# Kernel tuning notes

Hardware: AMD Instinct MI355X
Metric: run time of the kernel (lower is better)

Reference implementation:

```python
import jax, jax.numpy as jnp
import numpy as np

EPS_LN = 1e-5
EPS_BN = 1e-5

B, S, N, F, H, E, L = 8, 16, 1024, 16, 128, 32768, 4


def _layernorm(h, g, b):
    mu = h.mean(-1, keepdims=True)
    var = ((h - mu) ** 2).mean(-1, keepdims=True)
    return (h - mu) / jnp.sqrt(var + EPS_LN) * g + b


def setup_inputs() -> dict:
    key = jax.random.key(0)
    ks = iter(jax.random.split(key, 40))
    nrm = lambda shape, s=0.05: jax.random.normal(next(ks), shape, dtype=jnp.float32) * s
    inp = {
        'x': jax.random.normal(next(ks), (B, S, N, F), dtype=jnp.float32),
        'edge_index': jax.random.randint(next(ks), (2, E), 0, N, dtype=jnp.int32),
        'edge_weights': jax.random.uniform(next(ks), (E,), dtype=jnp.float32),
        'edge_features': jax.random.normal(next(ks), (E, 1), dtype=jnp.float32),
        # input projection: Linear(F,H) + LayerNorm(H)
        'w_in': nrm((F, H), 1.0 / np.sqrt(F)), 'b_in': nrm((H,)),
        'ln_in_g': jnp.ones((H,), jnp.float32), 'ln_in_b': jnp.zeros((H,), jnp.float32),
        # edge feature proj: Linear(1,H) -> ReLU -> Linear(H,1) -> Sigmoid
        'w_e1': nrm((1, H), 1.0), 'b_e1': nrm((H,)),
        'w_e2': nrm((H, 1), 1.0 / np.sqrt(H)), 'b_e2': nrm((1,)),
        # L GCN layers (weight [H,H], bias [H]) + BatchNorm1d affine params
        'gcn_w': nrm((L, H, H), 1.0 / np.sqrt(H)), 'gcn_b': nrm((L, H)),
        'bn_g': jnp.ones((L, H), jnp.float32), 'bn_b': jnp.zeros((L, H), jnp.float32),
        # 2-layer LSTM (PyTorch gate order i,f,g,o)
        'lstm_wih': nrm((2, 4 * H, H), 1.0 / np.sqrt(H)), 'lstm_whh': nrm((2, 4 * H, H), 1.0 / np.sqrt(H)),
        'lstm_bih': nrm((2, 4 * H)), 'lstm_bhh': nrm((2, 4 * H)),
        # output projection: Linear(H,H//2) + LayerNorm + Linear(H//2,1)
        'w_o1': nrm((H, H // 2), 1.0 / np.sqrt(H)), 'b_o1': nrm((H // 2,)),
        'ln_o_g': jnp.ones((H // 2,), jnp.float32), 'ln_o_b': jnp.zeros((H // 2,), jnp.float32),
        'w_o2': nrm((H // 2, 1), 1.0 / np.sqrt(H // 2)), 'b_o2': nrm((1,)),
    }
    return inp


def _forward(x, edge_index, edge_weights, edge_features,
             w_in, b_in, ln_in_g, ln_in_b, w_e1, b_e1, w_e2, b_e2,
             gcn_w, gcn_b, bn_g, bn_b,
             lstm_wih, lstm_whh, lstm_bih, lstm_bhh,
             w_o1, b_o1, ln_o_g, ln_o_b, w_o2, b_o2):
    Bs, Ss, Ns, Fs = x.shape
    BN = Bs * Ns
    # edge attention gating of edge weights
    e = jax.nn.relu(edge_features @ w_e1 + b_e1)
    att = jax.nn.sigmoid(e @ w_e2 + b_e2)[:, 0]            # [E]
    ew = edge_weights * att
    # input projection (dropout = identity in eval)
    h0 = jax.nn.relu(_layernorm(x @ w_in + b_in, ln_in_g, ln_in_b))   # [B,S,N,H]
    xf = h0.reshape(Bs * Ss, Ns, H)
    # replicate original slicing x[t:t+B] on the flattened (B*S) axis
    idx = jnp.arange(Ss)[:, None] + jnp.arange(Bs)[None, :]           # [S,B]
    hs = xf[idx].reshape(Ss, BN, H)                                   # [S,B*N,H]
    # GCN normalization (shared across timesteps): self-loops over all B*N nodes
    src = jnp.concatenate([edge_index[0], jnp.arange(BN, dtype=edge_index.dtype)])
    dst = jnp.concatenate([edge_index[1], jnp.arange(BN, dtype=edge_index.dtype)])
    w_sl = jnp.concatenate([ew, jnp.ones((BN,), ew.dtype)])
    deg = jax.ops.segment_sum(w_sl, dst, num_segments=BN)
    dis = jnp.where(deg > 0, jax.lax.rsqrt(jnp.where(deg > 0, deg, 1.0)), 0.0)
    norm = dis[src] * w_sl * dis[dst]                                  # [E+BN]
    # eval-mode BatchNorm (running mean 0, var 1)
    bn_scale = bn_g / np.sqrt(1.0 + EPS_BN)

    def gcn_block(h):                                                  # [BN,H]
        for l in range(L):
            identity = h
            hw = h @ gcn_w[l]
            m = jax.ops.segment_sum(hw[src] * norm[:, None], dst, num_segments=BN) + gcn_b[l]
            h = jax.nn.relu(m * bn_scale[l] + bn_b[l]) + identity
        return h

    hs = jax.vmap(gcn_block)(hs)                                       # [S,B*N,H]
    xt = jnp.transpose(hs.reshape(Ss, Bs, Ns, H), (1, 0, 2, 3))        # [B,S,N,H]
    # LSTM over the time axis for each (b,n) node sequence
    seq = jnp.transpose(xt, (0, 2, 1, 3)).reshape(BN, Ss, H)           # [B*N,S,H]

    def lstm_layer(seq, wih, whh, bih, bhh):
        def step(carry, xt):
            hprev, cprev = carry
            gates = xt @ wih.T + hprev @ whh.T + bih + bhh
            i, f, g, o = jnp.split(gates, 4, axis=-1)
            c = jax.nn.sigmoid(f) * cprev + jax.nn.sigmoid(i) * jnp.tanh(g)
            hn = jax.nn.sigmoid(o) * jnp.tanh(c)
            return (hn, c), hn
        z = jnp.zeros((seq.shape[0], H), seq.dtype)
        _, ys = jax.lax.scan(step, (z, z), jnp.swapaxes(seq, 0, 1))
        return jnp.swapaxes(ys, 0, 1)                                  # [B*N,S,H]

    y = lstm_layer(seq, lstm_wih[0], lstm_whh[0], lstm_bih[0], lstm_bhh[0])
    y = lstm_layer(y, lstm_wih[1], lstm_whh[1], lstm_bih[1], lstm_bhh[1])
    y = y[:, -1].reshape(Bs, Ns, H)
    z = jax.nn.relu(_layernorm(y @ w_o1 + b_o1, ln_o_g, ln_o_b))
    out = z @ w_o2 + b_o2                                              # [B,N,1]
    return out[..., None]                                              # [B,N,1,1]


def reference(x, edge_index, edge_weights, edge_features,
              w_in, b_in, ln_in_g, ln_in_b, w_e1, b_e1, w_e2, b_e2,
              gcn_w, gcn_b, bn_g, bn_b,
              lstm_wih, lstm_whh, lstm_bih, lstm_bhh,
              w_o1, b_o1, ln_o_g, ln_o_b, w_o2, b_o2):
    return _forward(x, edge_index, edge_weights, edge_features,
                    w_in, b_in, ln_in_g, ln_in_b, w_e1, b_e1, w_e2, b_e2,
                    gcn_w, gcn_b, bn_g, bn_b,
                    lstm_wih, lstm_whh, lstm_bih, lstm_bhh,
                    w_o1, b_o1, ln_o_g, ln_o_b, w_o2, b_o2)
```

## Files before the change

kernel.cpp:

```cpp
#include <hip/hip_runtime.h>
#include <cstdint>

#define EPS 1e-5f

typedef unsigned short ushort_t;
typedef __bf16 bf16x8 __attribute__((ext_vector_type(8)));
typedef float f32x4 __attribute__((ext_vector_type(4)));

#define GLD16(gp, lp) __builtin_amdgcn_global_load_lds( \
    (const __attribute__((address_space(1))) void*)(gp), \
    (__attribute__((address_space(3))) void*)(lp), 16, 0, 0)

__device__ __forceinline__ float sigm(float x) { return 1.f / (1.f + expf(-x)); }
__device__ __forceinline__ unsigned short f2bf(float f) {
    unsigned int u = __builtin_bit_cast(unsigned int, f);
    return (unsigned short)((u + 0x7fffu + ((u >> 16) & 1u)) >> 16);
}
__device__ __forceinline__ float bf2f(unsigned short s) {
    unsigned int u = ((unsigned int)s) << 16;
    return __builtin_bit_cast(float, u);
}
__device__ __forceinline__ float sigm_fast(float x) {
    float t = __builtin_amdgcn_exp2f(-1.44269504f * x);
    return __builtin_amdgcn_rcpf(1.f + t);
}
__device__ __forceinline__ float tanh_fast(float x) {
    float xc = fminf(fmaxf(x, -15.f), 15.f);
    float t = __builtin_amdgcn_exp2f(-2.88539008f * xc);
    return (1.f - t) * __builtin_amdgcn_rcpf(1.f + t);
}

__global__ __launch_bounds__(256) void edge_att_deg(const float* __restrict__ ef,
                                                    const float* __restrict__ we1,
                                                    const float* __restrict__ be1,
                                                    const float* __restrict__ we2,
                                                    const float* __restrict__ be2,
                                                    const float* __restrict__ ewin,
                                                    const int* __restrict__ dst,
                                                    float* __restrict__ ew,
                                                    float* __restrict__ deg) {
    int e = blockIdx.x * blockDim.x + threadIdx.x;
    if (e >= 32768) return;
    float x = ef[e];
    float acc = 0.f;
    for (int h = 0; h < 128; ++h) {
        float v = fmaxf(x * we1[h] + be1[h], 0.f);
        acc += v * we2[h];
    }
    float wv = ewin[e] * sigm(acc + be2[0]);
    ew[e] = wv;
    atomicAdd(&deg[dst[e]], wv);
}
__global__ __launch_bounds__(256) void make_dis(float* __restrict__ deg) {
    int i = blockIdx.x * blockDim.x + threadIdx.x;
    if (i < 1024) { float d = deg[i] + 1.0f; deg[i] = (d > 0.f) ? rsqrtf(d) : 0.f; }
}
__global__ __launch_bounds__(256) void scatterA(const int* __restrict__ src,
                                                const int* __restrict__ dst,
                                                const float* __restrict__ ew,
                                                const float* __restrict__ dis,
                                                float* __restrict__ A) {
    int e = blockIdx.x * blockDim.x + threadIdx.x;
    if (e >= 32768) return;
    int s = src[e], d = dst[e];
    atomicAdd(&A[d * 1024 + s], dis[s] * ew[e] * dis[d]);
}

__global__ __launch_bounds__(256) void convF2B(const float* __restrict__ s,
                                               ushort_t* __restrict__ d, int n) {
    int i = blockIdx.x * blockDim.x + threadIdx.x;
    if (i < n) d[i] = f2bf(s[i]);
}
__global__ __launch_bounds__(256) void conv_all(const float* __restrict__ gcnw,
                                                const float* __restrict__ wih,
                                                const float* __restrict__ whh,
                                                const float* __restrict__ bih,
                                                const float* __restrict__ bhh,
                                                ushort_t* __restrict__ gcnwT,
                                                ushort_t* __restrict__ wgi,
                                                ushort_t* __restrict__ wgh,
                                                float* __restrict__ bsg) {
    int i = blockIdx.x * 256 + threadIdx.x;
    if (i < 65536) {
        int l = i >> 14, rem = i & 16383, in = rem >> 7, outc = rem & 127;
        gcnwT[l * 16384 + outc * 128 + in] = f2bf(gcnw[i]);
        return;
    }
    int j = i - 65536;
    if (j < 131072) {
        int l = j >> 16, rem = j & 65535, c = rem >> 7, kx = rem & 127;
        int g = (c >> 4) & 3, h = (c >> 6) * 16 + (c & 15);
        int src = (l * 512 + g * 128 + h) * 128 + kx;
        wgi[j] = f2bf(wih[src]);
        wgh[j] = f2bf(whh[src]);
        return;
    }
    int b = j - 131072;
    if (b < 1024) {
        int l = b >> 9, c = b & 511;
        int g = (c >> 4) & 3, h = (c >> 6) * 16 + (c & 15);
        int src = l * 512 + g * 128 + h;
        bsg[b] = bih[src] + bhh[src];
    }
}

__global__ __launch_bounds__(256) void in_proj_ln(const float* __restrict__ x,
                                                  const float* __restrict__ w,
                                                  const float* __restrict__ bias,
                                                  const float* __restrict__ g,
                                                  const float* __restrict__ be,
                                                  ushort_t* __restrict__ hA,
                                                  ushort_t* __restrict__ hB) {
    int row = blockIdx.x * 4 + (threadIdx.x >> 6);
    int lane = threadIdx.x & 63;
    int k = row >> 10, n = row & 1023;
    float xv = x[(int64_t)row * 16 + (lane & 15)];
    float a0 = bias[lane], a1 = bias[lane + 64];
#pragma unroll
    for (int f = 0; f < 16; ++f) {
        float xf = __shfl(xv, f, 16);
        a0 += xf * w[f * 128 + lane];
        a1 += xf * w[f * 128 + lane + 64];
    }
    float s = a0 + a1;
#pragma unroll
    for (int off = 1; off < 64; off <<= 1) s += __shfl_xor(s, off, 64);
    float mu = s * (1.f / 128.f);
    float d0 = a0 - mu, d1 = a1 - mu;
    float vs = d0 * d0 + d1 * d1;
#pragma unroll
    for (int off = 1; off < 64; off <<= 1) vs += __shfl_xor(vs, off, 64);
    float rstd = rsqrtf(vs * (1.f / 128.f) + EPS);
    float v0 = fmaxf(d0 * rstd * g[lane] + be[lane], 0.f);
    float v1 = fmaxf(d1 * rstd * g[lane + 64] + be[lane + 64], 0.f);
    int64_t idx = ((int64_t)k * 1024 + n) * 128 + lane;
    ushort_t b0 = f2bf(v0), b1v = f2bf(v1);
    if (k < 16) { hA[idx] = b0; hA[idx + 64] = b1v; }
    hB[idx] = b0; hB[idx + 64] = b1v;
}

__global__ __launch_bounds__(256) void gemm_feat_t(const ushort_t* __restrict__ hA,
                                                   const ushort_t* __restrict__ Wt,
                                                   ushort_t* __restrict__ hwT) {
    __shared__ __align__(16) char AsB[32768];
    __shared__ __align__(16) char BsB[32768];
    const int tid = threadIdx.x, lane = tid & 63, wid = tid >> 6;
    const int wr = wid >> 1, wc = wid & 1, q = lane >> 4, l15 = lane & 15;
    const int t = blockIdx.y;
    const int row0 = blockIdx.x * 128;
    const ushort_t* Ap = hA + ((int64_t)t * 1024 + row0) * 128;
    f32x4 acc[4][4];
#pragma unroll
    for (int m = 0; m < 4; ++m)
#pragma unroll
        for (int n = 0; n < 4; ++n) acc[m][n] = f32x4{0.f, 0.f, 0.f, 0.f};
#pragma unroll
    for (int i = 0; i < 8; ++i) {
        int id = i * 256 + tid; int r = id >> 4, sg = id & 15;
        uint4 va = *(const uint4*)(Ap + r * 128 + sg * 8);
        *(uint4*)(AsB + r * 256 + ((sg * 16) ^ ((r & 7) << 4))) = va;
        uint4 vb = *(const uint4*)(Wt + r * 128 + sg * 8);
        *(uint4*)(BsB + r * 256 + ((sg * 16) ^ ((r & 7) << 4))) = vb;
    }
    __syncthreads();
#pragma unroll
    for (int kk = 0; kk < 4; ++kk) {
        bf16x8 af[4], bfr[4];
#pragma unroll
        for (int m = 0; m < 4; ++m) {
            int row = wr * 64 + m * 16 + l15;
            af[m] = __builtin_bit_cast(bf16x8,
                *(const uint4*)(AsB + row * 256 + ((kk * 64 + q * 16) ^ ((row & 7) << 4))));
        }
#pragma unroll
        for (int n = 0; n < 4; ++n) {
            int col = wc * 64 + n * 16 + l15;
            bfr[n] = __builtin_bit_cast(bf16x8,
                *(const uint4*)(BsB + col * 256 + ((kk * 64 + q * 16) ^ ((col & 7) << 4))));
        }
#pragma unroll
        for (int m = 0; m < 4; ++m)
#pragma unroll
            for (int n = 0; n < 4; ++n)
                acc[m][n] = __builtin_amdgcn_mfma_f32_16x16x32_bf16(af[m], bfr[n], acc[m][n], 0, 0, 0);
    }
#pragma unroll
    for (int m = 0; m < 4; ++m) {
        int bn = row0 + wr * 64 + m * 16 + q * 4;
#pragma unroll
        for (int n = 0; n < 4; ++n) {
            int col = wc * 64 + n * 16 + l15;
            ushort4 u;
            u.x = f2bf(acc[m][n][0]); u.y = f2bf(acc[m][n][1]);
            u.z = f2bf(acc[m][n][2]); u.w = f2bf(acc[m][n][3]);
            *(ushort4*)(hwT + ((int64_t)t * 128 + col) * 1024 + bn) = u;
        }
    }
}

__global__ __launch_bounds__(256) void gcn_layer(ushort_t* __restrict__ hA,
                                                 ushort_t* __restrict__ hB,
                                                 const ushort_t* __restrict__ Wt,
                                                 const ushort_t* __restrict__ Abf,
                                                 const ushort_t* __restrict__ hwT,
                                                 const float* __restrict__ dis,
                                                 const float* __restrict__ gcnb,
                                                 const float* __restrict__ bng,
                                                 const float* __restrict__ bnb) {
    __shared__ __align__(16) char AsB[16384];
    __shared__ __align__(16) char BsB[32768];
    const int tid = threadIdx.x, lane = tid & 63, wid = tid >> 6;
    const int wr = wid >> 1, wc = wid & 1, q = lane >> 4, l15 = lane & 15;
    const int bx = blockIdx.x;
    const bool adj = bx < 256;
    const int lb = adj ? bx : bx - 256;
    const int tt = lb >> 4;
    const int n0 = (lb & 15) * 64;
    ushort_t* Ap = (adj ? hA : hB) + ((int64_t)tt * 1024 + n0) * 128;

#pragma unroll
    for (int i = 0; i < 4; ++i) {
        int id = i * 256 + tid; int r = id >> 4, sg = id & 15;
        uint4 va = *(const uint4*)(Ap + r * 128 + sg * 8);
        *(uint4*)(AsB + r * 256 + ((sg * 16) ^ ((r & 7) << 4))) = va;
    }
#pragma unroll
    for (int i = 0; i < 8; ++i) {
        int id = i * 256 + tid; int r = id >> 4, sg = id & 15;
        uint4 vb = *(const uint4*)(Wt + r * 128 + sg * 8);
        *(uint4*)(BsB + r * 256 + ((sg * 16) ^ ((r & 7) << 4))) = vb;
    }
    __syncthreads();

    f32x4 accF[2][4];
#pragma unroll
    for (int m = 0; m < 2; ++m)
#pragma unroll
        for (int n = 0; n < 4; ++n) accF[m][n] = f32x4{0.f, 0.f, 0.f, 0.f};
#pragma unroll
    for (int kk = 0; kk < 4; ++kk) {
        bf16x8 af[2], bfr[4];
#pragma unroll
        for (int m = 0; m < 2; ++m) {
            int row = wr * 32 + m * 16 + l15;
            af[m] = __builtin_bit_cast(bf16x8,
                *(const uint4*)(AsB + row * 256 + ((kk * 64 + q * 16) ^ ((row & 7) << 4))));
        }
#pragma unroll
        for (int n = 0; n < 4; ++n) {
            int col = wc * 64 + n * 16 + l15;
            bfr[n] = __builtin_bit_cast(bf16x8,
                *(const uint4*)(BsB + col * 256 + ((kk * 64 + q * 16) ^ ((col & 7) << 4))));
        }
#pragma unroll
        for (int m = 0; m < 2; ++m)
#pragma unroll
            for (int n = 0; n < 4; ++n)
                accF[m][n] = __builtin_amdgcn_mfma_f32_16x16x32_bf16(af[m], bfr[n], accF[m][n], 0, 0, 0);
    }

    f32x4 accA[2][4];
#pragma unroll
    for (int m = 0; m < 2; ++m)
#pragma unroll
        for (int n = 0; n < 4; ++n) accA[m][n] = f32x4{0.f, 0.f, 0.f, 0.f};
    if (adj) {
        const int rl8 = lane >> 3;
        const int sgg = (lane & 7) ^ rl8;
        for (int k0 = 0; k0 < 1024; k0 += 64) {
            __syncthreads();
#pragma unroll
            for (int i = 0; i < 2; ++i) {
                int r = i * 32 + wid * 8 + rl8;
                GLD16(Abf + (int64_t)(n0 + r) * 1024 + k0 + sgg * 8,
                      BsB + (i * 32 + wid * 8) * 128);
            }
#pragma unroll
            for (int i = 0; i < 4; ++i) {
                int r = i * 32 + wid * 8 + rl8;
                GLD16(hwT + (int64_t)tt * 131072 + (int64_t)r * 1024 + k0 + sgg * 8,
                      BsB + 8192 + (i * 32 + wid * 8) * 128);
            }
            __syncthreads();
#pragma unroll
            for (int kk = 0; kk < 2; ++kk) {
                bf16x8 af2[2], bf2[4];
#pragma unroll
                for (int m = 0; m < 2; ++m) {
                    int row = wr * 32 + m * 16 + l15;
                    af2[m] = __builtin_bit_cast(bf16x8,
                        *(const uint4*)(BsB + row * 128 + ((kk * 64 + q * 16) ^ ((row & 7) << 4))));
                }
#pragma unroll
                for (int n = 0; n < 4; ++n) {
                    int col = wc * 64 + n * 16 + l15;
                    bf2[n] = __builtin_bit_cast(bf16x8,
                        *(const uint4*)(BsB + 8192 + col * 128 + ((kk * 64 + q * 16) ^ ((col & 7) << 4))));
                }
#pragma unroll
                for (int m = 0; m < 2; ++m)
#pragma unroll
                    for (int n = 0; n < 4; ++n)
                        accA[m][n] = __builtin_amdgcn_mfma_f32_16x16x32_bf16(af2[m], bf2[n], accA[m][n], 0, 0, 0);
            }
        }
    }
    __syncthreads();

    const float rs = rsqrtf(1.f + EPS);
#pragma unroll
    for (int n = 0; n < 4; ++n) {
        int col = wc * 64 + n * 16 + l15;
        float gb = gcnb[col], sc = bng[col] * rs, bb = bnb[col];
        int seg16 = (col >> 3) * 16, wb = (col & 7) * 2;
#pragma unroll
        for (int m = 0; m < 2; ++m) {
            int rl0 = wr * 32 + m * 16 + q * 4;
#pragma unroll
            for (int e = 0; e < 4; ++e) {
                int rl = rl0 + e;
                float sl = 1.f, ad = 0.f;
                if (adj) { float dv = dis[n0 + rl]; sl = dv * dv; ad = accA[m][n][e]; }
                float mv = sl * accF[m][n][e] + gb + ad;
                ushort_t rbv = *(const ushort_t*)(AsB + rl * 256 + (seg16 ^ ((rl & 7) << 4)) + wb);
                float v = fmaxf(mv * sc + bb, 0.f) + bf2f(rbv);
                *(ushort_t*)(BsB + rl * 256 + (seg16 ^ ((rl & 7) << 4)) + wb) = f2bf(v);
            }
        }
    }
    __syncthreads();
#pragma unroll
    for (int i = 0; i < 4; ++i) {
        int id = i * 256 + tid; int r = id >> 4, sg = id & 15;
        uint4 v = *(const uint4*)(BsB + r * 256 + ((sg * 16) ^ ((r & 7) << 4)));
        *(uint4*)(Ap + r * 128 + sg * 8) = v;
    }
}

template <int MODE>
__global__ __launch_bounds__(512, 2) void lstm_layer(
    const ushort_t* __restrict__ hA, const ushort_t* __restrict__ hB,
    const ushort_t* __restrict__ X,
    const ushort_t* __restrict__ Wi, const ushort_t* __restrict__ Wh,
    const float* __restrict__ bs,
    ushort_t* __restrict__ Y,
    const float* __restrict__ w1, const float* __restrict__ b1,
    const float* __restrict__ lg, const float* __restrict__ lb,
    const float* __restrict__ w2, const float* __restrict__ b2,
    float* __restrict__ out) {
    __shared__ __align__(16) char Xs[16384];
    __shared__ __align__(16) char Hs[16384];
    __shared__ __align__(16) char W1s[32768];
    const int tid = threadIdx.x, lane = tid & 63, w = tid >> 6;
    const int q = lane >> 4, l15 = lane & 15;
    const int row0 = blockIdx.x * 32;
    const int r = tid >> 4, sg = tid & 15;
    const int bb = row0 >> 10, n0 = row0 & 1023;

    *(uint4*)(Hs + tid * 16) = uint4{0, 0, 0, 0};
    if constexpr (MODE == 1) {
#pragma unroll
        for (int i = 0; i < 4; ++i)
            *(uint4*)(W1s + (i * 512 + tid) * 16) =
                *(const uint4*)((const char*)w1 + (i * 512 + tid) * 16);
    }
    bf16x8 wi[4][4], wh[4][4];
#pragma unroll
    for (int n = 0; n < 4; ++n)
#pragma unroll
        for (int kk = 0; kk < 4; ++kk) {
            int col = w * 64 + n * 16 + l15;
            wi[n][kk] = __builtin_bit_cast(bf16x8, *(const uint4*)(Wi + col * 128 + kk * 32 + q * 8));
            wh[n][kk] = __builtin_bit_cast(bf16x8, *(const uint4*)(Wh + col * 128 + kk * 32 + q * 8));
        }
    const int cb = w * 64 + l15;
    const float bi = bs[cb], bf = bs[cb + 16], bg = bs[cb + 32], bo = bs[cb + 48];
    const int k = w * 16 + l15;
    float c[2][4] = {};

    auto xsrc = [&](int t) -> const ushort_t* {
        if constexpr (MODE == 0)
            return (bb == 0) ? hA + ((int64_t)t * 1024 + n0) * 128
                             : hB + ((int64_t)(t + bb) * 1024 + n0) * 128;
        else
            return X + ((int64_t)t * 8192 + row0) * 128;
    };

    {
        uint4 x0 = *(const uint4*)(xsrc(0) + r * 128 + sg * 8);
        *(uint4*)(Xs + r * 256 + ((sg * 16) ^ ((r & 7) << 4))) = x0;
    }
    __syncthreads();

    for (int t = 0; t < 16; ++t) {
        const int p = (t & 1) * 8192, pn = ((t + 1) & 1) * 8192;
        uint4 xn;
        if (t < 15) xn = *(const uint4*)(xsrc(t + 1) + r * 128 + sg * 8);

        f32x4 acc[2][4];
#pragma unroll
        for (int m = 0; m < 2; ++m)
#pragma unroll
            for (int n = 0; n < 4; ++n) acc[m][n] = f32x4{0.f, 0.f, 0.f, 0.f};
#pragma unroll
        for (int kk = 0; kk < 4; ++kk) {
            bf16x8 ax[2], ah[2];
#pragma unroll
            for (int m = 0; m < 2; ++m) {
                int rw = m * 16 + l15;
                int off = rw * 256 + ((kk * 64 + q * 16) ^ ((rw & 7) << 4));
                ax[m] = __builtin_bit_cast(bf16x8, *(const uint4*)(Xs + p + off));
                ah[m] = __builtin_bit_cast(bf16x8, *(const uint4*)(Hs + p + off));
            }
#pragma unroll
            for (int n = 0; n < 4; ++n)
#pragma unroll
                for (int m = 0; m < 2; ++m) {
                    acc[m][n] = __builtin_amdgcn_mfma_f32_16x16x32_bf16(ax[m], wi[n][kk], acc[m][n], 0, 0, 0);
                    acc[m][n] = __builtin_amdgcn_mfma_f32_16x16x32_bf16(ah[m], wh[n][kk], acc[m][n], 0, 0, 0);
                }
        }
#pragma unroll
        for (int m = 0; m < 2; ++m)
#pragma unroll
            for (int e = 0; e < 4; ++e) {
                float ig = sigm_fast(acc[m][0][e] + bi);
                float fg = sigm_fast(acc[m][1][e] + bf);
                float gg = tanh_fast(acc[m][2][e] + bg);
                float og = sigm_fast(acc[m][3][e] + bo);
                float cn = fg * c[m][e] + ig * gg;
                c[m][e] = cn;
                float hn = og * tanh_fast(cn);
                int rw = m * 16 + q * 4 + e;
                int byte = rw * 256 + ((((k >> 3) * 16) ^ ((rw & 7) << 4)) | ((k & 7) * 2));
                *(ushort_t*)(Hs + pn + byte) = f2bf(hn);
            }
        if (t < 15)
            *(uint4*)(Xs + pn + r * 256 + ((sg * 16) ^ ((r & 7) << 4))) = xn;
        __syncthreads();

        if constexpr (MODE == 0) {
            uint4 v = *(const uint4*)(Hs + pn + r * 256 + ((sg * 16) ^ ((r & 7) << 4)));
            *(uint4*)(Y + ((int64_t)t * 8192 + row0 + r) * 128 + sg * 8) = v;
        }
    }

    if constexpr (MODE == 1) {
        float accj[4] = {b1[sg * 4 + 0], b1[sg * 4 + 1], b1[sg * 4 + 2], b1[sg * 4 + 3]};
#pragma unroll
        for (int kb = 0; kb < 16; ++kb) {
            uint4 hv = *(const uint4*)(Hs + r * 256 + ((kb * 16) ^ ((r & 7) << 4)));
            const ushort_t* hp = (const ushort_t*)&hv;
#pragma unroll
            for (int j2 = 0; j2 < 8; ++j2) {
                float hval = bf2f(hp[j2]);
                int kx = kb * 8 + j2;
                f32x4 wv = *(const f32x4*)(W1s + kx * 256 + sg * 16);
                accj[0] += hval * wv[0]; accj[1] += hval * wv[1];
                accj[2] += hval * wv[2]; accj[3] += hval * wv[3];
            }
        }
        float s4 = accj[0] + accj[1] + accj[2] + accj[3];
        s4 += __shfl_xor(s4, 1); s4 += __shfl_xor(s4, 2);
        s4 += __shfl_xor(s4, 4); s4 += __shfl_xor(s4, 8);
        float mu = s4 * (1.f / 64.f);
        float d0 = accj[0] - mu, d1 = accj[1] - mu, d2 = accj[2] - mu, d3 = accj[3] - mu;
        float v4 = d0 * d0 + d1 * d1 + d2 * d2 + d3 * d3;
        v4 += __shfl_xor(v4, 1); v4 += __shfl_xor(v4, 2);
        v4 += __shfl_xor(v4, 4); v4 += __shfl_xor(v4, 8);
        float rstd = rsqrtf(v4 * (1.f / 64.f) + EPS);
        float dj[4] = {d0, d1, d2, d3};
        float p2 = 0.f;
#pragma unroll
        for (int j = 0; j < 4; ++j) {
            int jj = sg * 4 + j;
            float z = fmaxf(dj[j] * rstd * lg[jj] + lb[jj], 0.f);
            p2 += z * w2[jj];
        }
        p2 += __shfl_xor(p2, 1); p2 += __shfl_xor(p2, 2);
        p2 += __shfl_xor(p2, 4); p2 += __shfl_xor(p2, 8);
        if (sg == 0) out[row0 + r] = p2 + b2[0];
    }
}

extern "C" void kernel_launch(void* const* d_in, const int* in_sizes, int n_in,
                              void* d_out, int out_size, void* d_ws, size_t ws_size,
                              hipStream_t stream) {
    const float* x    = (const float*)d_in[0];
    const int*   eidx = (const int*)d_in[1];
    const float* ewt  = (const float*)d_in[2];
    const float* efeat= (const float*)d_in[3];
    const float* w_in = (const float*)d_in[4];
    const float* b_in = (const float*)d_in[5];
    const float* lng  = (const float*)d_in[6];
    const float* lnb  = (const float*)d_in[7];
    const float* we1  = (const float*)d_in[8];
    const float* be1  = (const float*)d_in[9];
    const float* we2  = (const float*)d_in[10];
    const float* be2  = (const float*)d_in[11];
    const float* gcnw = (const float*)d_in[12];
    const float* gcnb = (const float*)d_in[13];
    const float* bng  = (const float*)d_in[14];
    const float* bnb  = (const float*)d_in[15];
    const float* wih  = (const float*)d_in[16];
    const float* whh  = (const float*)d_in[17];
    const float* bih  = (const float*)d_in[18];
    const float* bhh  = (const float*)d_in[19];
    const float* wo1  = (const float*)d_in[20];
    const float* bo1  = (const float*)d_in[21];
    const float* lnog = (const float*)d_in[22];
    const float* lnob = (const float*)d_in[23];
    const float* wo2  = (const float*)d_in[24];
    const float* bo2  = (const float*)d_in[25];
    float* out = (float*)d_out;

    char* W = (char*)d_ws;
    ushort_t* hA        = (ushort_t*)(W);
    ushort_t* hB        = (ushort_t*)(W + (4ll << 20));
    ushort_t* y1        = (ushort_t*)(W + (10ll << 20));
    ushort_t* hwT       = (ushort_t*)(W + (42ll << 20));
    float*    Adense    = (float*)(W + (46ll << 20));
    ushort_t* Adense_bf = (ushort_t*)(W + (50ll << 20));
    float*    ew        = (float*)(W + (52ll << 20));
    float*    dis       = (float*)(W + (52ll << 20) + 0x20000);
    float*    bsg       = (float*)(W + (52ll << 20) + 0x21000);
    ushort_t* gcnwT     = (ushort_t*)(W + (52ll << 20) + 0x22000);
    ushort_t* wgi       = (ushort_t*)(W + (52ll << 20) + 0x42000);
    ushort_t* wgh       = (ushort_t*)(W + (52ll << 20) + 0x82000);

    const int* srcI = eidx;
    const int* dstI = eidx + 32768;

    hipMemsetAsync(dis, 0, 1024 * sizeof(float), stream);
    hipMemsetAsync(Adense, 0, 1048576 * sizeof(float), stream);
    edge_att_deg<<<128, 256, 0, stream>>>(efeat, we1, be1, we2, be2, ewt, dstI, ew, dis);
    make_dis<<<4, 256, 0, stream>>>(dis);
    scatterA<<<128, 256, 0, stream>>>(srcI, dstI, ew, dis, Adense);
    convF2B<<<4096, 256, 0, stream>>>(Adense, Adense_bf, 1048576);
    conv_all<<<772, 256, 0, stream>>>(gcnw, wih, whh, bih, bhh, gcnwT, wgi, wgh, bsg);

    in_proj_ln<<<5888, 256, 0, stream>>>(x, w_in, b_in, lng, lnb, hA, hB);

    for (int l = 0; l < 4; ++l) {
        gemm_feat_t<<<dim3(8, 16, 1), 256, 0, stream>>>(hA, gcnwT + l * 16384, hwT);
        gcn_layer<<<624, 256, 0, stream>>>(hA, hB, gcnwT + l * 16384, Adense_bf, hwT,
                                           dis, gcnb + l * 128, bng + l * 128, bnb + l * 128);
    }

    lstm_layer<0><<<256, 512, 0, stream>>>(hA, hB, nullptr, wgi, wgh, bsg, y1,
                                           nullptr, nullptr, nullptr, nullptr,
                                           nullptr, nullptr, nullptr);
    lstm_layer<1><<<256, 512, 0, stream>>>(nullptr, nullptr, y1,
                                           wgi + 65536, wgh + 65536, bsg + 512, nullptr,
                                           wo1, bo1, lnog, lnob, wo2, bo2, out);
}
```

Before: 247.7 us.

## Fuse both LSTM layers into one pipelined kernel with per-block flags

Replaces the two sequential LSTM layer launches with a single 512-block launch. The first 256 blocks run layer 1 and publish a per-block timestep counter after writing each step's output. The other 256 blocks run layer 2 and spin on those counters, so the second layer can start before the first finishes. This overlaps the two recurrences and removes one launch. It relies on all 512 blocks being co-resident to avoid deadlock, hence the occupancy hint is raised to 4. It also adds atomic polling and an extra block-wide barrier on every producer step.

```diff
diff --git a/kernel.cpp b/kernel.cpp
--- a/kernel.cpp
+++ b/kernel.cpp
@@ -337,33 +337,36 @@
     }
 }
 
-template <int MODE>
-__global__ __launch_bounds__(512, 2) void lstm_layer(
+__global__ __launch_bounds__(512, 4) void lstm_pipe(
     const ushort_t* __restrict__ hA, const ushort_t* __restrict__ hB,
-    const ushort_t* __restrict__ X,
-    const ushort_t* __restrict__ Wi, const ushort_t* __restrict__ Wh,
-    const float* __restrict__ bs,
-    ushort_t* __restrict__ Y,
+    ushort_t* __restrict__ y1,
+    const ushort_t* __restrict__ wgi, const ushort_t* __restrict__ wgh,
+    const float* __restrict__ bsg,
     const float* __restrict__ w1, const float* __restrict__ b1,
     const float* __restrict__ lg, const float* __restrict__ lb,
     const float* __restrict__ w2, const float* __restrict__ b2,
-    float* __restrict__ out) {
+    float* __restrict__ out, int* __restrict__ flags) {
     __shared__ __align__(16) char Xs[16384];
     __shared__ __align__(16) char Hs[16384];
     __shared__ __align__(16) char W1s[32768];
     const int tid = threadIdx.x, lane = tid & 63, w = tid >> 6;
     const int q = lane >> 4, l15 = lane & 15;
-    const int row0 = blockIdx.x * 32;
+    const bool prod = blockIdx.x < 256;
+    const int b = prod ? blockIdx.x : blockIdx.x - 256;
+    const int row0 = b * 32;
     const int r = tid >> 4, sg = tid & 15;
     const int bb = row0 >> 10, n0 = row0 & 1023;
 
     *(uint4*)(Hs + tid * 16) = uint4{0, 0, 0, 0};
-    if constexpr (MODE == 1) {
+    if (!prod) {
 #pragma unroll
         for (int i = 0; i < 4; ++i)
             *(uint4*)(W1s + (i * 512 + tid) * 16) =
                 *(const uint4*)((const char*)w1 + (i * 512 + tid) * 16);
     }
+    const ushort_t* Wi = wgi + (prod ? 0 : 65536);
+    const ushort_t* Wh = wgh + (prod ? 0 : 65536);
+    const float*    bs = bsg + (prod ? 0 : 512);
     bf16x8 wi[4][4], wh[4][4];
 #pragma unroll
     for (int n = 0; n < 4; ++n)
@@ -379,13 +382,22 @@
     float c[2][4] = {};
 
     auto xsrc = [&](int t) -> const ushort_t* {
-        if constexpr (MODE == 0)
+        if (prod)
             return (bb == 0) ? hA + ((int64_t)t * 1024 + n0) * 128
                              : hB + ((int64_t)(t + bb) * 1024 + n0) * 128;
         else
-            return X + ((int64_t)t * 8192 + row0) * 128;
+            return y1 + ((int64_t)t * 8192 + row0) * 128;
     };
-
+    auto waitflag = [&](int need) {
+        if (tid == 0) {
+            while (__hip_atomic_load(flags + b, __ATOMIC_RELAXED, __HIP_MEMORY_SCOPE_AGENT) < need)
+                __builtin_amdgcn_s_sleep(8);
+            (void)__hip_atomic_load(flags + b, __ATOMIC_ACQUIRE, __HIP_MEMORY_SCOPE_AGENT);
+        }
+        __syncthreads();
+    };
+
+    if (!prod) waitflag(1);
     {
         uint4 x0 = *(const uint4*)(xsrc(0) + r * 128 + sg * 8);
         *(uint4*)(Xs + r * 256 + ((sg * 16) ^ ((r & 7) << 4))) = x0;
@@ -395,7 +407,10 @@
     for (int t = 0; t < 16; ++t) {
         const int p = (t & 1) * 8192, pn = ((t + 1) & 1) * 8192;
         uint4 xn;
-        if (t < 15) xn = *(const uint4*)(xsrc(t + 1) + r * 128 + sg * 8);
+        if (t < 15) {
+            if (!prod) waitflag(t + 2);
+            xn = *(const uint4*)(xsrc(t + 1) + r * 128 + sg * 8);
+        }
 
         f32x4 acc[2][4];
 #pragma unroll
@@ -439,13 +454,16 @@
             *(uint4*)(Xs + pn + r * 256 + ((sg * 16) ^ ((r & 7) << 4))) = xn;
         __syncthreads();
 
-        if constexpr (MODE == 0) {
+        if (prod) {
             uint4 v = *(const uint4*)(Hs + pn + r * 256 + ((sg * 16) ^ ((r & 7) << 4)));
-            *(uint4*)(Y + ((int64_t)t * 8192 + row0 + r) * 128 + sg * 8) = v;
-        }
-    }
-
-    if constexpr (MODE == 1) {
+            *(uint4*)(y1 + ((int64_t)t * 8192 + row0 + r) * 128 + sg * 8) = v;
+            __syncthreads();
+            if (tid == 0)
+                __hip_atomic_store(flags + b, t + 1, __ATOMIC_RELEASE, __HIP_MEMORY_SCOPE_AGENT);
+        }
+    }
+
+    if (!prod) {
         float accj[4] = {b1[sg * 4 + 0], b1[sg * 4 + 1], b1[sg * 4 + 2], b1[sg * 4 + 3]};
 #pragma unroll
         for (int kb = 0; kb < 16; ++kb) {
@@ -527,12 +545,14 @@
     ushort_t* gcnwT     = (ushort_t*)(W + (52ll << 20) + 0x22000);
     ushort_t* wgi       = (ushort_t*)(W + (52ll << 20) + 0x42000);
     ushort_t* wgh       = (ushort_t*)(W + (52ll << 20) + 0x82000);
+    int*      flags     = (int*)(W + (52ll << 20) + 0xC2000);
 
     const int* srcI = eidx;
     const int* dstI = eidx + 32768;
 
     hipMemsetAsync(dis, 0, 1024 * sizeof(float), stream);
     hipMemsetAsync(Adense, 0, 1048576 * sizeof(float), stream);
+    hipMemsetAsync(flags, 0, 256 * sizeof(int), stream);
     edge_att_deg<<<128, 256, 0, stream>>>(efeat, we1, be1, we2, be2, ewt, dstI, ew, dis);
     make_dis<<<4, 256, 0, stream>>>(dis);
     scatterA<<<128, 256, 0, stream>>>(srcI, dstI, ew, dis, Adense);
@@ -547,10 +567,6 @@
                                            dis, gcnb + l * 128, bng + l * 128, bnb + l * 128);
     }
 
-    lstm_layer<0><<<256, 512, 0, stream>>>(hA, hB, nullptr, wgi, wgh, bsg, y1,
-                                           nullptr, nullptr, nullptr, nullptr,
-                                           nullptr, nullptr, nullptr);
-    lstm_layer<1><<<256, 512, 0, stream>>>(nullptr, nullptr, y1,
-                                           wgi + 65536, wgh + 65536, bsg + 512, nullptr,
-                                           wo1, bo1, lnog, lnob, wo2, bo2, out);
-}
+    lstm_pipe<<<512, 512, 0, stream>>>(hA, hB, y1, wgi, wgh, bsg,
+                                       wo1, bo1, lnog, lnob, wo2, bo2, out, flags);
+}
```

Result: slower. 622.0 us (+151.1%).
